# Performance work log

Hardware: AMD Instinct MI355X
Metric: run time of the kernel (lower is better)

Reference implementation:

```python
import jax, jax.numpy as jnp
import numpy as np

SEQ_LEN = 512
INPUT_DIM = 128
NUM_HIDDEN = 1024
NUM_CLASSES = 128
BATCH = 256


def setup_inputs() -> dict:
    key = jax.random.key(0)
    ks = jax.random.split(key, 10)
    std = 0.01
    d, h, c = INPUT_DIM, NUM_HIDDEN, NUM_CLASSES
    inp = {
        'x': jax.random.randint(ks[0], (BATCH, SEQ_LEN), 0, INPUT_DIM, dtype=jnp.int32),
        'W_xg': jax.random.normal(ks[1], (d, h), jnp.float32) * std,
        'W_hg': jax.random.normal(ks[2], (h, h), jnp.float32) * std,
        'b_g': jnp.zeros((h,), jnp.float32),
        'W_xi': jax.random.normal(ks[3], (d, h), jnp.float32) * std,
        'W_hi': jax.random.normal(ks[4], (h, h), jnp.float32) * std,
        'b_i': jnp.zeros((h,), jnp.float32),
        'W_xf': jax.random.normal(ks[5], (d, h), jnp.float32) * std,
        'W_hf': jax.random.normal(ks[6], (h, h), jnp.float32) * std,
        'b_f': jnp.zeros((h,), jnp.float32),
        'W_xo': jax.random.normal(ks[7], (d, h), jnp.float32) * std,
        'W_ho': jax.random.normal(ks[8], (h, h), jnp.float32) * std,
        'b_o': jnp.zeros((h,), jnp.float32),
        'W_hp': jax.random.normal(ks[9], (h, c), jnp.float32) * std,
        'b_p': jnp.zeros((c,), jnp.float32),
    }
    return inp


def reference(x, W_xg, W_hg, b_g, W_xi, W_hi, b_i, W_xf, W_hf, b_f,
              W_xo, W_ho, b_o, W_hp, b_p):
    B = x.shape[0]
    # Precompute one-hot input projections for all timesteps via gather:
    # x_t @ W_x* == W_x*[x_t] since x_t is one-hot. Shapes: [B, T, H]
    xg = W_xg[x]
    xi = W_xi[x]
    xf = W_xf[x]
    xo = W_xo[x]

    def step(carry, inputs):
        h, c = carry
        xg_t, xi_t, xf_t, xo_t = inputs  # each [B, H]
        g = jnp.tanh(xg_t + h @ W_hg + b_g)
        i = jax.nn.sigmoid(xi_t + h @ W_hi + b_i)
        f = jax.nn.sigmoid(xf_t + h @ W_hf + b_f)
        o = jax.nn.sigmoid(xo_t + h @ W_ho + b_o)
        c = g * i + c * f
        h = jnp.tanh(c) * o
        return (h, c), None

    h0 = jnp.zeros((B, NUM_HIDDEN), x_dtype := xg.dtype)
    c0 = jnp.zeros((B, NUM_HIDDEN), x_dtype)
    # scan over time: transpose precomputed projections to [T, B, H]
    seq = (jnp.swapaxes(xg, 0, 1), jnp.swapaxes(xi, 0, 1),
           jnp.swapaxes(xf, 0, 1), jnp.swapaxes(xo, 0, 1))
    (h, c), _ = jax.lax.scan(step, (h0, c0), seq)
    return h @ W_hp + b_p
```

## Files before the change

### kernel.cpp

```cpp
#include <hip/hip_runtime.h>
#include <stdint.h>

#define BATCH 256
#define SEQT  512
#define HID   1024
#define NCLS  128

using bf16x8 = __attribute__((ext_vector_type(8))) short;
using f32x4  = __attribute__((ext_vector_type(4))) float;
using i32x2  = __attribute__((ext_vector_type(2))) int;

__device__ __forceinline__ unsigned short f2bf(float x) {
    unsigned u = __float_as_uint(x);
    u = u + 0x7FFFu + ((u >> 16) & 1u);
    return (unsigned short)(u >> 16);
}
__device__ __forceinline__ float bf2f(unsigned short s) {
    return __uint_as_float(((unsigned)s) << 16);
}
__device__ __forceinline__ float sigf(float x) { return 1.f / (1.f + __expf(-x)); }
__device__ __forceinline__ float tanhf_(float x) {
    x = fminf(12.f, fmaxf(-12.f, x));
    float e = __expf(2.f * x);
    return (e - 1.f) / (e + 1.f);
}

__device__ __forceinline__ void ld_a_sc1(bf16x8& d, const unsigned short* p) {
    asm volatile("global_load_dwordx4 %0, %1, off sc1" : "=v"(d) : "v"(p));
}

__device__ __forceinline__ unsigned ag_load(unsigned* p) {
    return __hip_atomic_load(p, __ATOMIC_RELAXED, __HIP_MEMORY_SCOPE_AGENT);
}
__device__ __forceinline__ void ag_store(unsigned* p, unsigned v) {
    __hip_atomic_store(p, v, __ATOMIC_RELAXED, __HIP_MEMORY_SCOPE_AGENT);
}
__device__ __forceinline__ unsigned ag_add(unsigned* p) {
    return __hip_atomic_fetch_add(p, 1u, __ATOMIC_RELAXED, __HIP_MEMORY_SCOPE_AGENT);
}

__global__ void xtrans_kernel(const int* __restrict__ x, int* __restrict__ xT) {
    int b = blockIdx.x;
    for (int t = threadIdx.x; t < SEQT; t += 256) xT[t * BATCH + b] = x[b * SEQT + t];
}

__global__ void __launch_bounds__(256, 2) lstm_pers(
    const int* __restrict__ xT,
    const float* __restrict__ Wxg, const float* __restrict__ Whg, const float* __restrict__ b_g,
    const float* __restrict__ Wxi, const float* __restrict__ Whi, const float* __restrict__ b_i,
    const float* __restrict__ Wxf, const float* __restrict__ Whf, const float* __restrict__ b_f,
    const float* __restrict__ Wxo, const float* __restrict__ Who, const float* __restrict__ b_o,
    unsigned short* __restrict__ hbuf, unsigned int* __restrict__ cnt,
    unsigned int* __restrict__ misc)
{
    extern __shared__ char lds[];
    const int tid = threadIdx.x;
    const int w   = tid >> 6;
    const int l   = tid & 63;
    const int lHi = l >> 4;
    const int lLo = l & 15;

    volatile int* bailp = (volatile int*)(lds + 12288);
    volatile int* bcast = (volatile int*)(lds + 12292);
    unsigned* abortf  = misc + 0;
    unsigned* gticket = misc + 16;

    if (tid == 0) {
        *bailp = 0;
        bcast[0] = (int)ag_add(gticket);
    }
    __syncthreads();
    const int slot  = bcast[0];
    const int panel = slot >> 6;
    const int r0    = panel * 32;
    const int hu0   = (slot & 63) * 16;

    bf16x8 B0[8][4];
#pragma unroll
    for (int kk = 0; kk < 8; ++kk) {
#pragma unroll
        for (int g = 0; g < 4; ++g) {
            const float* Wsrc = (g == 0) ? Whg : (g == 1) ? Whi : (g == 2) ? Whf : Who;
            const size_t kb = (size_t)((w << 8) + kk * 32 + (lHi << 3));
#pragma unroll
            for (int e = 0; e < 8; ++e)
                B0[kk][g][e] = (short)f2bf(Wsrc[(kb + e) * HID + hu0 + lLo]);
        }
    }

    const int hu = hu0 + lLo;
    const float vbg = b_g[hu], vbi = b_i[hu], vbf = b_f[hu], vbo = b_o[hu];

    char* pb = lds;
    const int fm  = w >> 1;
    const int fhf = w & 1;
    float cst[2] = {0.f, 0.f};
    const int frow = r0 + fm * 16 + (lHi << 2) + 2 * fhf;

    unsigned* addline  = cnt + ((panel * 8 + (slot & 7)) << 4);
    unsigned* pollline = cnt + ((panel * 8 + (l & 7)) << 4);

    float xw[4][2];
    {
        i32x2 idx = *(const i32x2*)(xT + 0 * BATCH + frow);
#pragma unroll
        for (int rr = 0; rr < 2; ++rr) {
            xw[0][rr] = Wxg[(size_t)idx[rr] * HID + hu];
            xw[1][rr] = Wxi[(size_t)idx[rr] * HID + hu];
            xw[2][rr] = Wxf[(size_t)idx[rr] * HID + hu];
            xw[3][rr] = Wxo[(size_t)idx[rr] * HID + hu];
        }
    }

    for (int t = 0; t < SEQT; ++t) {
        const unsigned short* cur = hbuf + (size_t)(t & 1) * BATCH * HID;
        unsigned short*       nxt = hbuf + (size_t)((t + 1) & 1) * BATCH * HID;

        const unsigned short* a0 = cur + (size_t)(r0 + lLo) * HID + ((w << 8) + (lHi << 3));
        const unsigned short* a1 = a0 + 16 * HID;

        f32x4 acc[2][4];
#pragma unroll
        for (int m = 0; m < 2; ++m)
#pragma unroll
            for (int g = 0; g < 4; ++g) acc[m][g] = (f32x4){0.f, 0.f, 0.f, 0.f};

        bf16x8 pf[4][2];
        ld_a_sc1(pf[0][0], a0 + 0 * 32);  ld_a_sc1(pf[0][1], a1 + 0 * 32);
        ld_a_sc1(pf[1][0], a0 + 1 * 32);  ld_a_sc1(pf[1][1], a1 + 1 * 32);
        ld_a_sc1(pf[2][0], a0 + 2 * 32);  ld_a_sc1(pf[2][1], a1 + 2 * 32);
#pragma unroll
        for (int kk = 0; kk < 8; ++kk) {
            if (kk < 5) {
                ld_a_sc1(pf[(kk + 3) & 3][0], a0 + (kk + 3) * 32);
                ld_a_sc1(pf[(kk + 3) & 3][1], a1 + (kk + 3) * 32);
            }
            if      (kk < 5)  asm volatile("s_waitcnt vmcnt(6)" ::: "memory");
            else if (kk == 5) asm volatile("s_waitcnt vmcnt(4)" ::: "memory");
            else if (kk == 6) asm volatile("s_waitcnt vmcnt(2)" ::: "memory");
            else              asm volatile("s_waitcnt vmcnt(0)" ::: "memory");
            __builtin_amdgcn_sched_barrier(0);
#pragma unroll
            for (int g = 0; g < 4; ++g) {
                acc[0][g] = __builtin_amdgcn_mfma_f32_16x16x32_bf16(pf[kk & 3][0], B0[kk][g], acc[0][g], 0, 0, 0);
                acc[1][g] = __builtin_amdgcn_mfma_f32_16x16x32_bf16(pf[kk & 3][1], B0[kk][g], acc[1][g], 0, 0, 0);
            }
        }

        const int bailed = *bailp;
#pragma unroll
        for (int f = 0; f < 4; ++f) {
            if (f != w) {
                const int m_  = f >> 1;
                const int hf_ = f & 1;
                const int src = (w < f) ? w : (w - 1);
#pragma unroll
                for (int g = 0; g < 4; ++g) {
                    unsigned pk = (unsigned)f2bf(acc[m_][g][2 * hf_ + 0]) |
                                  ((unsigned)f2bf(acc[m_][g][2 * hf_ + 1]) << 16);
                    *(unsigned*)(pb + ((f * 3 + src) * 4 + g) * 256 + l * 4) = pk;
                }
            }
        }
        __syncthreads();

#pragma unroll
        for (int f = 0; f < 4; ++f) {
            if (w == f) {
                const int m_  = f >> 1;
                const int hf_ = f & 1;
                float pre[4][2];
#pragma unroll
                for (int g = 0; g < 4; ++g) {
                    pre[g][0] = acc[m_][g][2 * hf_ + 0];
                    pre[g][1] = acc[m_][g][2 * hf_ + 1];
#pragma unroll
                    for (int s = 0; s < 3; ++s) {
                        unsigned pk = *(const unsigned*)(pb + ((f * 3 + s) * 4 + g) * 256 + l * 4);
                        pre[g][0] += bf2f((unsigned short)(pk & 0xFFFFu));
                        pre[g][1] += bf2f((unsigned short)(pk >> 16));
                    }
                }
#pragma unroll
                for (int rr = 0; rr < 2; ++rr) {
                    float gg = tanhf_(pre[0][rr] + xw[0][rr] + vbg);
                    float ii = sigf  (pre[1][rr] + xw[1][rr] + vbi);
                    float ff = sigf  (pre[2][rr] + xw[2][rr] + vbf);
                    float oo = sigf  (pre[3][rr] + xw[3][rr] + vbo);
                    cst[rr] = gg * ii + cst[rr] * ff;
                    float hv = tanhf_(cst[rr]) * oo;
                    unsigned short hs = bailed ? (unsigned short)0x42C8 : f2bf(hv);
                    unsigned pk32 = (unsigned)hs;
                    unsigned oth  = (unsigned)__shfl_xor((int)pk32, 1, 64) & 0xFFFFu;
                    if ((lLo & 1) == 0) {
                        unsigned v32 = pk32 | (oth << 16);
                        unsigned* p32 = (unsigned*)&nxt[(size_t)(frow + rr) * HID + hu];
                        __hip_atomic_store(p32, v32, __ATOMIC_RELAXED, __HIP_MEMORY_SCOPE_AGENT);
                    }
                }
            }
        }
        __syncthreads();

        if (tid == 0) ag_add(addline);

        {
            const int tn = (t + 1 < SEQT) ? t + 1 : t;
            i32x2 idx = *(const i32x2*)(xT + tn * BATCH + frow);
#pragma unroll
            for (int rr = 0; rr < 2; ++rr) {
                xw[0][rr] = Wxg[(size_t)idx[rr] * HID + hu];
                xw[1][rr] = Wxi[(size_t)idx[rr] * HID + hu];
                xw[2][rr] = Wxf[(size_t)idx[rr] * HID + hu];
                xw[3][rr] = Wxo[(size_t)idx[rr] * HID + hu];
            }
        }

        if (w == 0 && !(*bailp)) {
            const unsigned target = 8u * (unsigned)(t + 1);
            unsigned guard = 0;
            bool ok = false;
            for (;;) {
                bool done = ag_load(pollline) >= target;
                if (__ballot(done) == ~0ull) { ok = true; break; }
                unsigned ab = ((guard & 63u) == 0u) ? ag_load(abortf) : 0u;
                if (ab) break;
                __builtin_amdgcn_s_sleep(1);
                if (++guard > (1u << 17)) {
                    if (l == 0) ag_store(abortf, 1u);
                    break;
                }
            }
            if (!ok && l == 0) *bailp = 1;
        }
        __syncthreads();
    }
}

__global__ void __launch_bounds__(256, 1) proj_kernel(
    const unsigned short* __restrict__ h, const float* __restrict__ Whp,
    const float* __restrict__ bp, float* __restrict__ out)
{
    __shared__ float red[4][256];
    const int tid  = threadIdx.x;
    const int n    = tid & 127;
    const int half = tid >> 7;
    const int b0   = blockIdx.x * 4;
    float s0 = 0.f, s1 = 0.f, s2 = 0.f, s3 = 0.f;
    for (int k = half * 512; k < half * 512 + 512; ++k) {
        float wv = Whp[(size_t)k * NCLS + n];
        s0 += bf2f(h[(size_t)(b0 + 0) * HID + k]) * wv;
        s1 += bf2f(h[(size_t)(b0 + 1) * HID + k]) * wv;
        s2 += bf2f(h[(size_t)(b0 + 2) * HID + k]) * wv;
        s3 += bf2f(h[(size_t)(b0 + 3) * HID + k]) * wv;
    }
    red[0][tid] = s0; red[1][tid] = s1; red[2][tid] = s2; red[3][tid] = s3;
    __syncthreads();
    if (tid < 128) {
#pragma unroll
        for (int j = 0; j < 4; ++j)
            out[(size_t)(b0 + j) * NCLS + tid] = red[j][tid] + red[j][tid + 128] + bp[tid];
    }
}

extern "C" void kernel_launch(void* const* d_in, const int* in_sizes, int n_in,
                              void* d_out, int out_size, void* d_ws, size_t ws_size,
                              hipStream_t stream) {
    const int*   x   = (const int*)  d_in[0];
    const float* Wxg = (const float*)d_in[1];
    const float* Whg = (const float*)d_in[2];
    const float* b_g = (const float*)d_in[3];
    const float* Wxi = (const float*)d_in[4];
    const float* Whi = (const float*)d_in[5];
    const float* b_i = (const float*)d_in[6];
    const float* Wxf = (const float*)d_in[7];
    const float* Whf = (const float*)d_in[8];
    const float* b_f = (const float*)d_in[9];
    const float* Wxo = (const float*)d_in[10];
    const float* Who = (const float*)d_in[11];
    const float* b_o = (const float*)d_in[12];
    const float* Whp = (const float*)d_in[13];
    const float* b_p = (const float*)d_in[14];
    float* out = (float*)d_out;

    char* ws = (char*)d_ws;
    unsigned short* hbuf = (unsigned short*)ws;
    int*            xT   = (int*)(ws + (1 << 20));
    unsigned int*   cnt  = (unsigned int*)(ws + (1 << 20) + (512*1024));
    unsigned int*   misc = cnt + 64 * 16;

    hipMemsetAsync(hbuf, 0, (size_t)BATCH * HID * sizeof(unsigned short), stream);
    hipMemsetAsync(cnt, 0, (size_t)(64 * 16 + 32) * sizeof(unsigned int), stream);

    xtrans_kernel<<<256, 256, 0, stream>>>(x, xT);

    const int ldsBytes = 12288 + 64;
    (void)hipFuncSetAttribute((const void*)lstm_pers,
                              hipFuncAttributeMaxDynamicSharedMemorySize, ldsBytes);
    lstm_pers<<<512, 256, ldsBytes, stream>>>(xT, Wxg, Whg, b_g, Wxi, Whi, b_i,
                                              Wxf, Whf, b_f, Wxo, Who, b_o, hbuf, cnt, misc);

    proj_kernel<<<64, 256, 0, stream>>>(hbuf, Whp, b_p, out);
}
```

Measured before the change: 3.462 ms.

## Move half of the recurrent weight fragments from registers to LDS, issue all A loads upfront

```diff
diff --git a/kernel.cpp b/kernel.cpp
--- a/kernel.cpp
+++ b/kernel.cpp
@@ -60,8 +60,9 @@
     const int lHi = l >> 4;
     const int lLo = l & 15;
 
-    volatile int* bailp = (volatile int*)(lds + 12288);
-    volatile int* bcast = (volatile int*)(lds + 12292);
+    char* pb = lds + 65536;
+    volatile int* bailp = (volatile int*)(lds + 77824);
+    volatile int* bcast = (volatile int*)(lds + 77828);
     unsigned* abortf  = misc + 0;
     unsigned* gticket = misc + 16;
 
@@ -75,9 +76,9 @@
     const int r0    = panel * 32;
     const int hu0   = (slot & 63) * 16;
 
-    bf16x8 B0[8][4];
-#pragma unroll
-    for (int kk = 0; kk < 8; ++kk) {
+    bf16x8 B0[4][4];
+#pragma unroll
+    for (int kk = 0; kk < 4; ++kk) {
 #pragma unroll
         for (int g = 0; g < 4; ++g) {
             const float* Wsrc = (g == 0) ? Whg : (g == 1) ? Whi : (g == 2) ? Whf : Who;
@@ -87,11 +88,23 @@
                 B0[kk][g][e] = (short)f2bf(Wsrc[(kb + e) * HID + hu0 + lLo]);
         }
     }
+#pragma unroll
+    for (int kk2 = 0; kk2 < 4; ++kk2) {
+#pragma unroll
+        for (int g = 0; g < 4; ++g) {
+            const float* Wsrc = (g == 0) ? Whg : (g == 1) ? Whi : (g == 2) ? Whf : Who;
+            const size_t kb = (size_t)((w << 8) + (kk2 + 4) * 32 + (lHi << 3));
+            bf16x8 v;
+#pragma unroll
+            for (int e = 0; e < 8; ++e)
+                v[e] = (short)f2bf(Wsrc[(kb + e) * HID + hu0 + lLo]);
+            *(bf16x8*)(lds + (w << 14) + ((kk2 * 4 + g) << 10) + (l << 4)) = v;
+        }
+    }
 
     const int hu = hu0 + lLo;
     const float vbg = b_g[hu], vbi = b_i[hu], vbf = b_f[hu], vbo = b_o[hu];
 
-    char* pb = lds;
     const int fm  = w >> 1;
     const int fhf = w & 1;
     float cst[2] = {0.f, 0.f};
@@ -125,25 +138,43 @@
 #pragma unroll
             for (int g = 0; g < 4; ++g) acc[m][g] = (f32x4){0.f, 0.f, 0.f, 0.f};
 
-        bf16x8 pf[4][2];
-        ld_a_sc1(pf[0][0], a0 + 0 * 32);  ld_a_sc1(pf[0][1], a1 + 0 * 32);
-        ld_a_sc1(pf[1][0], a0 + 1 * 32);  ld_a_sc1(pf[1][1], a1 + 1 * 32);
-        ld_a_sc1(pf[2][0], a0 + 2 * 32);  ld_a_sc1(pf[2][1], a1 + 2 * 32);
+        bf16x8 pf[8][2];
 #pragma unroll
         for (int kk = 0; kk < 8; ++kk) {
-            if (kk < 5) {
-                ld_a_sc1(pf[(kk + 3) & 3][0], a0 + (kk + 3) * 32);
-                ld_a_sc1(pf[(kk + 3) & 3][1], a1 + (kk + 3) * 32);
-            }
-            if      (kk < 5)  asm volatile("s_waitcnt vmcnt(6)" ::: "memory");
-            else if (kk == 5) asm volatile("s_waitcnt vmcnt(4)" ::: "memory");
-            else if (kk == 6) asm volatile("s_waitcnt vmcnt(2)" ::: "memory");
-            else              asm volatile("s_waitcnt vmcnt(0)" ::: "memory");
+            ld_a_sc1(pf[kk][0], a0 + kk * 32);
+            ld_a_sc1(pf[kk][1], a1 + kk * 32);
+        }
+#pragma unroll
+        for (int kk = 0; kk < 8; ++kk) {
+            bf16x8 bb[4];
+            if (kk >= 4) {
+#pragma unroll
+                for (int g = 0; g < 4; ++g)
+                    bb[g] = *(const bf16x8*)(lds + (w << 14) + (((kk - 4) * 4 + g) << 10) + (l << 4));
+            }
+            switch (kk) {
+                case 0: asm volatile("s_waitcnt vmcnt(14)" ::: "memory"); break;
+                case 1: asm volatile("s_waitcnt vmcnt(12)" ::: "memory"); break;
+                case 2: asm volatile("s_waitcnt vmcnt(10)" ::: "memory"); break;
+                case 3: asm volatile("s_waitcnt vmcnt(8)"  ::: "memory"); break;
+                case 4: asm volatile("s_waitcnt vmcnt(6)"  ::: "memory"); break;
+                case 5: asm volatile("s_waitcnt vmcnt(4)"  ::: "memory"); break;
+                case 6: asm volatile("s_waitcnt vmcnt(2)"  ::: "memory"); break;
+                default: asm volatile("s_waitcnt vmcnt(0)" ::: "memory"); break;
+            }
             __builtin_amdgcn_sched_barrier(0);
-#pragma unroll
-            for (int g = 0; g < 4; ++g) {
-                acc[0][g] = __builtin_amdgcn_mfma_f32_16x16x32_bf16(pf[kk & 3][0], B0[kk][g], acc[0][g], 0, 0, 0);
-                acc[1][g] = __builtin_amdgcn_mfma_f32_16x16x32_bf16(pf[kk & 3][1], B0[kk][g], acc[1][g], 0, 0, 0);
+            if (kk < 4) {
+#pragma unroll
+                for (int g = 0; g < 4; ++g) {
+                    acc[0][g] = __builtin_amdgcn_mfma_f32_16x16x32_bf16(pf[kk][0], B0[kk][g], acc[0][g], 0, 0, 0);
+                    acc[1][g] = __builtin_amdgcn_mfma_f32_16x16x32_bf16(pf[kk][1], B0[kk][g], acc[1][g], 0, 0, 0);
+                }
+            } else {
+#pragma unroll
+                for (int g = 0; g < 4; ++g) {
+                    acc[0][g] = __builtin_amdgcn_mfma_f32_16x16x32_bf16(pf[kk][0], bb[g], acc[0][g], 0, 0, 0);
+                    acc[1][g] = __builtin_amdgcn_mfma_f32_16x16x32_bf16(pf[kk][1], bb[g], acc[1][g], 0, 0, 0);
+                }
             }
         }
 
@@ -294,7 +325,7 @@
 
     xtrans_kernel<<<256, 256, 0, stream>>>(x, xT);
 
-    const int ldsBytes = 12288 + 64;
+    const int ldsBytes = 65536 + 12288 + 64;
     (void)hipFuncSetAttribute((const void*)lstm_pers,
                               hipFuncAttributeMaxDynamicSharedMemorySize, ldsBytes);
     lstm_pers<<<512, 256, ldsBytes, stream>>>(xT, Wxg, Whg, b_g, Wxi, Whi, b_i,
```

After: 3.645 ms. 1.05x slower.
